# Performance work log

Measured on AMD Instinct MI355X. Metric: run time of the kernel, lower is better.

Reference implementation:

```python
import jax, jax.numpy as jnp
import numpy as np

H = 16          # num query heads
G = 4           # num kv heads (groups)
MAX_POS = 128   # max relative position


def setup_inputs() -> dict:
    key = jax.random.key(0)
    ks = jax.random.split(key, 6)
    B, T, D = 8, 1024, 1024
    hd = D // H
    s = 0.02
    return {
        "x": jax.random.normal(ks[0], (B, T, D), jnp.float32),
        "Wq": jax.random.normal(ks[1], (D, D), jnp.float32) * s,
        "Wk": jax.random.normal(ks[2], (hd * G, D), jnp.float32) * s,
        "Wv": jax.random.normal(ks[3], (hd * G, D), jnp.float32) * s,
        "Wo": jax.random.normal(ks[4], (D, D), jnp.float32) * s,
        "E": jax.random.normal(ks[5], (2 * MAX_POS - 1, hd), jnp.float32) * s,
    }


def reference(x, Wq, Wk, Wv, Wo, E):
    B, T, D = x.shape
    hd = D // H
    r = H // G  # kv repeat factor

    # projections (torch nn.Linear convention: y = x @ W.T)
    q = (x @ Wq.T).reshape(B, T, H, hd).transpose(0, 2, 1, 3)  # [B,H,T,hd]
    k = (x @ Wk.T).reshape(B, T, G, hd)                         # [B,T,G,hd]
    v = (x @ Wv.T).reshape(B, T, G, hd)

    # GQA: query head h uses kv group h // r  (matches repeat_interleave)
    k = jnp.repeat(k, r, axis=2).transpose(0, 2, 1, 3)  # [B,H,T,hd]
    v = jnp.repeat(v, r, axis=2).transpose(0, 2, 1, 3)  # [B,H,T,hd]

    q = q * (1.0 / hd) ** 0.5
    scores = jnp.einsum("bhqd,bhkd->bhqk", q, k)  # [B,H,T,T]

    # relative position bias: R[i,j] = E[clamp(j - i) + MAX_POS - 1]
    pos = jnp.arange(T)
    dist = jnp.clip(pos[None, :] - pos[:, None], -MAX_POS + 1, MAX_POS - 1) + MAX_POS - 1
    R = E[dist]  # [T,T,hd]
    # original einsum 'bhd,thd->bht' with q=[B*H, Tq, hd], R=[Tk, Tq, hd]:
    # bias[b,h,q,kpos] = sum_d q[b,h,q,d] * R[kpos, q, d]
    bias = jnp.einsum("bhqd,kqd->bhqk", q, R)
    scores = scores + bias

    attn = jax.nn.softmax(scores, axis=-1)
    out = jnp.einsum("bhqk,bhkd->bhqd", attn, v)         # [B,H,T,hd]
    out = out.transpose(0, 2, 1, 3).reshape(B, T, D)      # [B,T,D]
    return out @ Wo.T
```

## Files before the change

kernel.cpp:

```cpp
#include <hip/hip_runtime.h>
#include <hip/hip_bf16.h>
#include <cstdint>
#include <cstddef>

typedef __hip_bfloat16 bf16;
typedef __attribute__((ext_vector_type(8))) __bf16 bf16x8;
typedef __attribute__((ext_vector_type(4))) float floatx4;

#define GPTR(p) ((const __attribute__((address_space(1))) void*)(p))
#define LPTR(p) ((__attribute__((address_space(3))) void*)(p))

__device__ __forceinline__ floatx4 mfma16(bf16x8 a, bf16x8 b, floatx4 c) {
  return __builtin_amdgcn_mfma_f32_16x16x32_bf16(a, b, c, 0, 0, 0);
}

__global__ __launch_bounds__(256) void cvt_bf16(const float* __restrict__ in,
                                                bf16* __restrict__ out, int n4) {
  for (int i = blockIdx.x * 256 + threadIdx.x; i < n4; i += gridDim.x * 256) {
    float4 v = ((const float4*)in)[i];
    alignas(8) bf16 t[4] = {__float2bfloat16(v.x), __float2bfloat16(v.y),
                            __float2bfloat16(v.z), __float2bfloat16(v.w)};
    *(uint64_t*)(out + (size_t)i * 4) = *(const uint64_t*)t;
  }
}

__global__ __launch_bounds__(256) void gemm_qkv(
    const bf16* __restrict__ A, const bf16* __restrict__ Wq,
    const bf16* __restrict__ Wk, const bf16* __restrict__ Wv,
    bf16* __restrict__ qout, bf16* __restrict__ kout,
    bf16* __restrict__ vTout) {
  __shared__ alignas(16) bf16 As[128 * 32];
  __shared__ alignas(16) bf16 Bs[128 * 32];
  const int tid = threadIdx.x;
  const int lane = tid & 63;
  const int w = tid >> 6;
  const int wr = w >> 1, wc = w & 1;
  const int quad = lane >> 4, c = lane & 15;
  const int m0 = blockIdx.y * 128;
  const int nb = blockIdx.x;

  int mode, nloc;
  const bf16* Wp;
  if (nb < 8) {
    mode = 1; Wp = Wq + (size_t)nb * 128 * 1024; nloc = nb * 128;
  } else if (nb < 10) {
    mode = 2; Wp = Wk + (size_t)(nb - 8) * 128 * 1024; nloc = (nb - 8) * 128;
  } else {
    mode = 3; Wp = Wv + (size_t)(nb - 10) * 128 * 1024; nloc = (nb - 10) * 128;
  }

  const int i0 = tid, i1 = tid + 256;
  const bf16* ga0 = A + (size_t)(m0 + (i0 >> 2)) * 1024 + (i0 & 3) * 8;
  const bf16* ga1 = A + (size_t)(m0 + (i1 >> 2)) * 1024 + (i1 & 3) * 8;
  const bf16* gb0 = Wp + (size_t)(i0 >> 2) * 1024 + (i0 & 3) * 8;
  const bf16* gb1 = Wp + (size_t)(i1 >> 2) * 1024 + (i1 & 3) * 8;

  floatx4 acc[4][4] = {};

  for (int kt = 0; kt < 32; ++kt) {
    if (kt) __syncthreads();
    __builtin_amdgcn_global_load_lds(GPTR(ga0), LPTR(&As[i0 * 8]), 16, 0, 0);
    __builtin_amdgcn_global_load_lds(GPTR(ga1), LPTR(&As[i1 * 8]), 16, 0, 0);
    __builtin_amdgcn_global_load_lds(GPTR(gb0), LPTR(&Bs[i0 * 8]), 16, 0, 0);
    __builtin_amdgcn_global_load_lds(GPTR(gb1), LPTR(&Bs[i1 * 8]), 16, 0, 0);
    ga0 += 32; ga1 += 32; gb0 += 32; gb1 += 32;
    __syncthreads();
    bf16x8 af[4], bfr[4];
#pragma unroll
    for (int i = 0; i < 4; ++i)
      af[i] = *(const bf16x8*)&As[(wr * 64 + i * 16 + c) * 32 + quad * 8];
#pragma unroll
    for (int j = 0; j < 4; ++j)
      bfr[j] = *(const bf16x8*)&Bs[(wc * 64 + j * 16 + c) * 32 + quad * 8];
#pragma unroll
    for (int i = 0; i < 4; ++i)
#pragma unroll
      for (int j = 0; j < 4; ++j)
        acc[i][j] = mfma16(af[i], bfr[j], acc[i][j]);
  }

  if (mode == 3) {
#pragma unroll
    for (int i = 0; i < 4; ++i)
#pragma unroll
      for (int j = 0; j < 4; ++j) {
        int m = m0 + wr * 64 + i * 16 + quad * 4;
        int n = nloc + wc * 64 + j * 16 + c;
        int b = m >> 10, t = m & 1023, g = n >> 6, d = n & 63;
        alignas(8) bf16 tmp[4];
#pragma unroll
        for (int r = 0; r < 4; ++r) tmp[r] = __float2bfloat16(acc[i][j][r]);
        *(uint64_t*)(vTout + (((size_t)(b * 4 + g)) * 64 + d) * 1024 + t) =
            *(const uint64_t*)tmp;
      }
    return;
  }

  const float scale = (mode == 1) ? 0.125f : 1.0f;
#pragma unroll
  for (int i = 0; i < 4; ++i)
#pragma unroll
    for (int j = 0; j < 4; ++j)
#pragma unroll
      for (int r = 0; r < 4; ++r) {
        int m = m0 + wr * 64 + i * 16 + quad * 4 + r;
        int n = nloc + wc * 64 + j * 16 + c;
        int b = m >> 10, t = m & 1023;
        bf16 v = __float2bfloat16(acc[i][j][r] * scale);
        if (mode == 1) {
          int h = n >> 6;
          qout[(((size_t)(b * 16 + h)) * 1024 + t) * 64 + (n & 63)] = v;
        } else {
          int g = n >> 6;
          kout[(((size_t)(b * 4 + g)) * 1024 + t) * 64 + (n & 63)] = v;
        }
      }
}

__global__ __launch_bounds__(256) void gemm_o(const bf16* __restrict__ A,
                                              const bf16* __restrict__ W,
                                              float* __restrict__ out) {
  __shared__ alignas(16) bf16 As[128 * 32];
  __shared__ alignas(16) bf16 Bs[128 * 32];
  const int tid = threadIdx.x;
  const int lane = tid & 63;
  const int w = tid >> 6;
  const int wr = w >> 1, wc = w & 1;
  const int quad = lane >> 4, c = lane & 15;
  const int m0 = blockIdx.y * 128, n0 = blockIdx.x * 128;

  const int i0 = tid, i1 = tid + 256;
  const bf16* ga0 = A + (size_t)(m0 + (i0 >> 2)) * 1024 + (i0 & 3) * 8;
  const bf16* ga1 = A + (size_t)(m0 + (i1 >> 2)) * 1024 + (i1 & 3) * 8;
  const bf16* gb0 = W + (size_t)(n0 + (i0 >> 2)) * 1024 + (i0 & 3) * 8;
  const bf16* gb1 = W + (size_t)(n0 + (i1 >> 2)) * 1024 + (i1 & 3) * 8;

  floatx4 acc[4][4] = {};

  for (int kt = 0; kt < 32; ++kt) {
    if (kt) __syncthreads();
    __builtin_amdgcn_global_load_lds(GPTR(ga0), LPTR(&As[i0 * 8]), 16, 0, 0);
    __builtin_amdgcn_global_load_lds(GPTR(ga1), LPTR(&As[i1 * 8]), 16, 0, 0);
    __builtin_amdgcn_global_load_lds(GPTR(gb0), LPTR(&Bs[i0 * 8]), 16, 0, 0);
    __builtin_amdgcn_global_load_lds(GPTR(gb1), LPTR(&Bs[i1 * 8]), 16, 0, 0);
    ga0 += 32; ga1 += 32; gb0 += 32; gb1 += 32;
    __syncthreads();
    bf16x8 af[4], bfr[4];
#pragma unroll
    for (int i = 0; i < 4; ++i)
      af[i] = *(const bf16x8*)&As[(wr * 64 + i * 16 + c) * 32 + quad * 8];
#pragma unroll
    for (int j = 0; j < 4; ++j)
      bfr[j] = *(const bf16x8*)&Bs[(wc * 64 + j * 16 + c) * 32 + quad * 8];
#pragma unroll
    for (int i = 0; i < 4; ++i)
#pragma unroll
      for (int j = 0; j < 4; ++j)
        acc[i][j] = mfma16(af[i], bfr[j], acc[i][j]);
  }

#pragma unroll
  for (int i = 0; i < 4; ++i)
#pragma unroll
    for (int j = 0; j < 4; ++j)
#pragma unroll
      for (int r = 0; r < 4; ++r) {
        int m = m0 + wr * 64 + i * 16 + quad * 4 + r;
        int n = n0 + wc * 64 + j * 16 + c;
        out[(size_t)m * 1024 + n] = acc[i][j][r];
      }
}

__device__ __forceinline__ void stage_tile_swz(const bf16* __restrict__ g,
                                               int gstride, bf16* __restrict__ dst,
                                               int tid) {
#pragma unroll
  for (int s = 0; s < 2; ++s) {
    int f = s * 256 + tid;
    int r = f >> 3, cb = f & 7;
    int cbg = cb ^ (r & 7);
    __builtin_amdgcn_global_load_lds(GPTR(g + (size_t)r * gstride + cbg * 8),
                                     LPTR(dst + f * 8), 16, 0, 0);
  }
}

__device__ __forceinline__ bf16x8 read_frag_swz(const bf16* __restrict__ tile,
                                                int row, int cb) {
  return *(const bf16x8*)&tile[row * 64 + ((cb ^ (row & 7)) * 8)];
}

__global__ __launch_bounds__(256, 3) void attn_kernel(
    const bf16* __restrict__ q_ws, const bf16* __restrict__ k_ws,
    const bf16* __restrict__ vT, const float* __restrict__ E,
    bf16* __restrict__ out) {
  __shared__ alignas(16) bf16 qEl[64 * 264];
  __shared__ alignas(16) bf16 Ks[64 * 72];
  __shared__ alignas(16) bf16 Vs[64 * 64];
  const int tid = threadIdx.x;
  const int lane = tid & 63, w = tid >> 6;
  const int quad = lane >> 4, c = lane & 15;
  const int bh = blockIdx.y;
  const int b = bh >> 4, h = bh & 15, g = h >> 2;
  const int qb = blockIdx.x * 64 + w * 16;

  const bf16* qrow = q_ws + ((size_t)bh * 1024 + qb + c) * 64;
  bf16x8 qf0 = *(const bf16x8*)(qrow + quad * 8);
  bf16x8 qf1 = *(const bf16x8*)(qrow + 32 + quad * 8);

  for (int jn = 0; jn < 16; ++jn) {
    int er = jn * 16 + c;
    er = er > 254 ? 254 : er;
    const float* Ep = E + (size_t)er * 64;
    float4 e0 = *(const float4*)(Ep + quad * 8);
    float4 e1 = *(const float4*)(Ep + quad * 8 + 4);
    float4 e2 = *(const float4*)(Ep + 32 + quad * 8);
    float4 e3 = *(const float4*)(Ep + 32 + quad * 8 + 4);
    alignas(16) bf16 t0b[8] = {
        __float2bfloat16(e0.x), __float2bfloat16(e0.y), __float2bfloat16(e0.z),
        __float2bfloat16(e0.w), __float2bfloat16(e1.x), __float2bfloat16(e1.y),
        __float2bfloat16(e1.z), __float2bfloat16(e1.w)};
    alignas(16) bf16 t1b[8] = {
        __float2bfloat16(e2.x), __float2bfloat16(e2.y), __float2bfloat16(e2.z),
        __float2bfloat16(e2.w), __float2bfloat16(e3.x), __float2bfloat16(e3.y),
        __float2bfloat16(e3.z), __float2bfloat16(e3.w)};
    floatx4 a = {};
    a = mfma16(qf0, *(const bf16x8*)t0b, a);
    a = mfma16(qf1, *(const bf16x8*)t1b, a);
#pragma unroll
    for (int r = 0; r < 4; ++r)
      qEl[(w * 16 + quad * 4 + r) * 264 + jn * 16 + c] = __float2bfloat16(a[r]);
  }

  const bf16* rowE = qEl + (size_t)(w * 16 + c) * 264;
  bf16* rowP = Ks + (size_t)(w * 16 + c) * 72;
  float mrow = -1e30f, lrow = 0.f;
  floatx4 o[4] = {};
  const bf16* kbase = k_ws + (size_t)(b * 4 + g) * 1024 * 64;
  const bf16* vbase = vT + (size_t)(b * 4 + g) * 64 * 1024;
  float blo = 0.f, bhi = 0.f;

  for (int t0 = 0; t0 < 1024; t0 += 64) {
    stage_tile_swz(kbase + (size_t)t0 * 64, 64, Ks, tid);
    stage_tile_swz(vbase + t0, 1024, Vs, tid);
    __syncthreads();
    if (t0 == 0) {
      blo = __bfloat162float(rowE[254]);
      bhi = __bfloat162float(rowE[0]);
    }
    floatx4 S[4];
#pragma unroll
    for (int j = 0; j < 4; ++j) {
      bf16x8 kf0 = read_frag_swz(Ks, j * 16 + c, quad);
      bf16x8 kf1 = read_frag_swz(Ks, j * 16 + c, quad + 4);
      floatx4 z = {};
      z = mfma16(kf0, qf0, z);
      S[j] = mfma16(kf1, qf1, z);
    }
    const int dlt0 = qb + c - t0;
    if (t0 <= qb - 190) {
#pragma unroll
      for (int j = 0; j < 4; ++j)
#pragma unroll
        for (int r = 0; r < 4; ++r) S[j][r] += blo;
    } else if (t0 >= qb + 142) {
#pragma unroll
      for (int j = 0; j < 4; ++j)
#pragma unroll
        for (int r = 0; r < 4; ++r) S[j][r] += bhi;
    } else {
#pragma unroll
      for (int j = 0; j < 4; ++j)
#pragma unroll
        for (int r = 0; r < 4; ++r) {
          int dlt = dlt0 - j * 16 - quad * 4 - r;
          dlt = dlt > 127 ? 127 : (dlt < -127 ? -127 : dlt);
          S[j][r] += __bfloat162float(rowE[dlt + 127]);
        }
    }
    float mx = -1e30f;
#pragma unroll
    for (int j = 0; j < 4; ++j)
#pragma unroll
      for (int r = 0; r < 4; ++r) mx = fmaxf(mx, S[j][r]);
    mx = fmaxf(mx, __shfl_xor(mx, 16, 64));
    mx = fmaxf(mx, __shfl_xor(mx, 32, 64));
    float nm = fmaxf(mrow, mx);
    float alpha = __expf(mrow - nm);
    float rs = 0.f;
#pragma unroll
    for (int j = 0; j < 4; ++j)
#pragma unroll
      for (int r = 0; r < 4; ++r) {
        float p = __expf(S[j][r] - nm);
        S[j][r] = p;
        rs += p;
      }
    rs += __shfl_xor(rs, 16, 64);
    rs += __shfl_xor(rs, 32, 64);
    lrow = lrow * alpha + rs;
    mrow = nm;
    __syncthreads();
#pragma unroll
    for (int j = 0; j < 4; ++j) {
      alignas(8) bf16 tmp[4];
#pragma unroll
      for (int r = 0; r < 4; ++r) tmp[r] = __float2bfloat16(S[j][r]);
      *(uint64_t*)(rowP + j * 16 + quad * 4) = *(const uint64_t*)tmp;
    }
    float av[4];
#pragma unroll
    for (int r = 0; r < 4; ++r) av[r] = __shfl(alpha, quad * 4 + r, 64);
#pragma unroll
    for (int jj = 0; jj < 4; ++jj)
#pragma unroll
      for (int r = 0; r < 4; ++r) o[jj][r] *= av[r];
    __threadfence_block();
    __builtin_amdgcn_wave_barrier();
    bf16x8 pf0 = *(const bf16x8*)(rowP + quad * 8);
    bf16x8 pf1 = *(const bf16x8*)(rowP + 32 + quad * 8);
#pragma unroll
    for (int jj = 0; jj < 4; ++jj) {
      bf16x8 vf0 = read_frag_swz(Vs, jj * 16 + c, quad);
      bf16x8 vf1 = read_frag_swz(Vs, jj * 16 + c, quad + 4);
      o[jj] = mfma16(pf0, vf0, o[jj]);
      o[jj] = mfma16(pf1, vf1, o[jj]);
    }
    __syncthreads();
  }

  float lr4[4];
#pragma unroll
  for (int r = 0; r < 4; ++r) lr4[r] = __shfl(lrow, quad * 4 + r, 64);
#pragma unroll
  for (int jj = 0; jj < 4; ++jj)
#pragma unroll
    for (int r = 0; r < 4; ++r) {
      int qi = qb + quad * 4 + r;
      out[(((size_t)b * 1024 + qi) * 16 + h) * 64 + jj * 16 + c] =
          __float2bfloat16(o[jj][r] / lr4[r]);
    }
}

extern "C" void kernel_launch(void* const* d_in, const int* in_sizes, int n_in,
                              void* d_out, int out_size, void* d_ws,
                              size_t ws_size, hipStream_t stream) {
  const float* x = (const float*)d_in[0];
  const float* Wq = (const float*)d_in[1];
  const float* Wk = (const float*)d_in[2];
  const float* Wv = (const float*)d_in[3];
  const float* Wo = (const float*)d_in[4];
  const float* E = (const float*)d_in[5];

  char* ws = (char*)d_ws;
  bf16* q_ws = (bf16*)d_out;
  bf16* x_bf = (bf16*)((char*)d_out + (16ull << 20));
  bf16* k_ws = (bf16*)(ws);
  bf16* vT = (bf16*)(ws + (4ull << 20));
  bf16* attn = (bf16*)(ws + (8ull << 20));
  bf16* Wq_bf = (bf16*)(ws + (8ull << 20));
  bf16* Wk_bf = (bf16*)(ws + (10ull << 20));
  bf16* Wv_bf = (bf16*)(ws + (10ull << 20) + (512ull << 10));
  bf16* Wo_bf = (bf16*)(ws);
  float* outp = (float*)d_out;

  cvt_bf16<<<2048, 256, 0, stream>>>(x, x_bf, 2097152);
  cvt_bf16<<<1024, 256, 0, stream>>>(Wq, Wq_bf, 262144);
  cvt_bf16<<<256, 256, 0, stream>>>(Wk, Wk_bf, 65536);
  cvt_bf16<<<256, 256, 0, stream>>>(Wv, Wv_bf, 65536);
  gemm_qkv<<<dim3(12, 64), 256, 0, stream>>>(x_bf, Wq_bf, Wk_bf, Wv_bf,
                                             q_ws, k_ws, vT);
  attn_kernel<<<dim3(16, 128), 256, 0, stream>>>(q_ws, k_ws, vT, E, attn);
  cvt_bf16<<<1024, 256, 0, stream>>>(Wo, Wo_bf, 262144);
  gemm_o<<<dim3(8, 64), 256, 0, stream>>>(attn, Wo_bf, outp);
}
```

Before: 285.6 us.

## Load K/V fragments directly from global memory into registers, drop LDS staging

Replaces the shared-memory staging of K and V tiles (global_load_lds with swizzle plus block barriers) with direct per-wave global loads of MFMA fragments into registers. P now gets its own small LDS buffer and the per-iteration __syncthreads are removed, so waves run independently. The cost is that each of the four waves redundantly fetches the same K/V tiles from global/L2, and the uncoalesced row-strided 16-byte loads may raise memory traffic and latency.

```diff
diff --git a/kernel.cpp b/kernel.cpp
--- a/kernel.cpp
+++ b/kernel.cpp
@@ -171,31 +171,12 @@
       }
 }
 
-__device__ __forceinline__ void stage_tile_swz(const bf16* __restrict__ g,
-                                               int gstride, bf16* __restrict__ dst,
-                                               int tid) {
-#pragma unroll
-  for (int s = 0; s < 2; ++s) {
-    int f = s * 256 + tid;
-    int r = f >> 3, cb = f & 7;
-    int cbg = cb ^ (r & 7);
-    __builtin_amdgcn_global_load_lds(GPTR(g + (size_t)r * gstride + cbg * 8),
-                                     LPTR(dst + f * 8), 16, 0, 0);
-  }
-}
-
-__device__ __forceinline__ bf16x8 read_frag_swz(const bf16* __restrict__ tile,
-                                                int row, int cb) {
-  return *(const bf16x8*)&tile[row * 64 + ((cb ^ (row & 7)) * 8)];
-}
-
 __global__ __launch_bounds__(256, 3) void attn_kernel(
     const bf16* __restrict__ q_ws, const bf16* __restrict__ k_ws,
     const bf16* __restrict__ vT, const float* __restrict__ E,
     bf16* __restrict__ out) {
   __shared__ alignas(16) bf16 qEl[64 * 264];
-  __shared__ alignas(16) bf16 Ks[64 * 72];
-  __shared__ alignas(16) bf16 Vs[64 * 64];
+  __shared__ alignas(16) bf16 Ps[64 * 72];
   const int tid = threadIdx.x;
   const int lane = tid & 63, w = tid >> 6;
   const int quad = lane >> 4, c = lane & 15;
@@ -230,31 +211,38 @@
     for (int r = 0; r < 4; ++r)
       qEl[(w * 16 + quad * 4 + r) * 264 + jn * 16 + c] = __float2bfloat16(a[r]);
   }
+  __syncthreads();
 
   const bf16* rowE = qEl + (size_t)(w * 16 + c) * 264;
-  bf16* rowP = Ks + (size_t)(w * 16 + c) * 72;
+  bf16* rowP = Ps + (size_t)(w * 16 + c) * 72;
   float mrow = -1e30f, lrow = 0.f;
   floatx4 o[4] = {};
   const bf16* kbase = k_ws + (size_t)(b * 4 + g) * 1024 * 64;
   const bf16* vbase = vT + (size_t)(b * 4 + g) * 64 * 1024;
-  float blo = 0.f, bhi = 0.f;
+  const float blo = __bfloat162float(rowE[254]);
+  const float bhi = __bfloat162float(rowE[0]);
 
   for (int t0 = 0; t0 < 1024; t0 += 64) {
-    stage_tile_swz(kbase + (size_t)t0 * 64, 64, Ks, tid);
-    stage_tile_swz(vbase + t0, 1024, Vs, tid);
-    __syncthreads();
-    if (t0 == 0) {
-      blo = __bfloat162float(rowE[254]);
-      bhi = __bfloat162float(rowE[0]);
+    bf16x8 kf[4][2];
+#pragma unroll
+    for (int j = 0; j < 4; ++j) {
+      const bf16* kr = kbase + (size_t)(t0 + j * 16 + c) * 64 + quad * 8;
+      kf[j][0] = *(const bf16x8*)kr;
+      kf[j][1] = *(const bf16x8*)(kr + 32);
     }
     floatx4 S[4];
 #pragma unroll
     for (int j = 0; j < 4; ++j) {
-      bf16x8 kf0 = read_frag_swz(Ks, j * 16 + c, quad);
-      bf16x8 kf1 = read_frag_swz(Ks, j * 16 + c, quad + 4);
       floatx4 z = {};
-      z = mfma16(kf0, qf0, z);
-      S[j] = mfma16(kf1, qf1, z);
+      z = mfma16(kf[j][0], qf0, z);
+      S[j] = mfma16(kf[j][1], qf1, z);
+    }
+    bf16x8 vf[4][2];
+#pragma unroll
+    for (int jj = 0; jj < 4; ++jj) {
+      const bf16* vr = vbase + (size_t)(jj * 16 + c) * 1024 + t0 + quad * 8;
+      vf[jj][0] = *(const bf16x8*)vr;
+      vf[jj][1] = *(const bf16x8*)(vr + 32);
     }
     const int dlt0 = qb + c - t0;
     if (t0 <= qb - 190) {
@@ -299,7 +287,6 @@
     rs += __shfl_xor(rs, 32, 64);
     lrow = lrow * alpha + rs;
     mrow = nm;
-    __syncthreads();
 #pragma unroll
     for (int j = 0; j < 4; ++j) {
       alignas(8) bf16 tmp[4];
@@ -320,12 +307,9 @@
     bf16x8 pf1 = *(const bf16x8*)(rowP + 32 + quad * 8);
 #pragma unroll
     for (int jj = 0; jj < 4; ++jj) {
-      bf16x8 vf0 = read_frag_swz(Vs, jj * 16 + c, quad);
-      bf16x8 vf1 = read_frag_swz(Vs, jj * 16 + c, quad + 4);
-      o[jj] = mfma16(pf0, vf0, o[jj]);
-      o[jj] = mfma16(pf1, vf1, o[jj]);
-    }
-    __syncthreads();
+      o[jj] = mfma16(pf0, vf[jj][0], o[jj]);
+      o[jj] = mfma16(pf1, vf[jj][1], o[jj]);
+    }
   }
 
   float lr4[4];
```

Result: slower. 445.8 us (+56.1%).

## Double-buffer K/V tiles in attention loop to overlap loads with compute

Applied to the files above, without the earlier changes.

Splits K and V shared buffers into two ping-pong copies and issues the async global-to-LDS load of the next tile before computing on the current one, so memory latency overlaps the MFMA and softmax work. The first tile is prefetched before the positional-bias precompute, and the loop is manually unrolled by two to swap buffers. It also lowers the launch-bounds occupancy hint from 3 to 2 blocks per CU to fit the extra shared memory. The last iteration wraps around and prefetches tile 0 needlessly, adding a little redundant traffic.

```diff
diff --git a/kernel.cpp b/kernel.cpp
--- a/kernel.cpp
+++ b/kernel.cpp
@@ -189,19 +189,124 @@
   return *(const bf16x8*)&tile[row * 64 + ((cb ^ (row & 7)) * 8)];
 }
 
-__global__ __launch_bounds__(256, 3) void attn_kernel(
+__device__ __forceinline__ void attn_tile(
+    int t0, const bf16* __restrict__ kbase, const bf16* __restrict__ vbase,
+    bf16* __restrict__ curK, bf16* __restrict__ nxtK,
+    bf16* __restrict__ curV, bf16* __restrict__ nxtV,
+    const bf16* __restrict__ rowE, int qb, int tid, int w, int quad, int c,
+    bf16x8 qf0, bf16x8 qf1, float blo, float bhi, float& mrow, float& lrow,
+    floatx4 (&o)[4]) {
+  const int nt0 = (t0 + 64) & 1023;
+  stage_tile_swz(vbase + nt0, 1024, nxtV, tid);
+  stage_tile_swz(kbase + (size_t)nt0 * 64, 64, nxtK, tid);
+  floatx4 S[4];
+#pragma unroll
+  for (int j = 0; j < 4; ++j) {
+    bf16x8 kf0 = read_frag_swz(curK, j * 16 + c, quad);
+    bf16x8 kf1 = read_frag_swz(curK, j * 16 + c, quad + 4);
+    floatx4 z = {};
+    z = mfma16(kf0, qf0, z);
+    S[j] = mfma16(kf1, qf1, z);
+  }
+  const int dlt0 = qb + c - t0;
+  if (t0 <= qb - 190) {
+#pragma unroll
+    for (int j = 0; j < 4; ++j)
+#pragma unroll
+      for (int r = 0; r < 4; ++r) S[j][r] += blo;
+  } else if (t0 >= qb + 142) {
+#pragma unroll
+    for (int j = 0; j < 4; ++j)
+#pragma unroll
+      for (int r = 0; r < 4; ++r) S[j][r] += bhi;
+  } else {
+#pragma unroll
+    for (int j = 0; j < 4; ++j)
+#pragma unroll
+      for (int r = 0; r < 4; ++r) {
+        int dlt = dlt0 - j * 16 - quad * 4 - r;
+        dlt = dlt > 127 ? 127 : (dlt < -127 ? -127 : dlt);
+        S[j][r] += __bfloat162float(rowE[dlt + 127]);
+      }
+  }
+  float mx = -1e30f;
+#pragma unroll
+  for (int j = 0; j < 4; ++j)
+#pragma unroll
+    for (int r = 0; r < 4; ++r) mx = fmaxf(mx, S[j][r]);
+  mx = fmaxf(mx, __shfl_xor(mx, 16, 64));
+  mx = fmaxf(mx, __shfl_xor(mx, 32, 64));
+  float nm = fmaxf(mrow, mx);
+  float alpha = __expf(mrow - nm);
+  float rs = 0.f;
+#pragma unroll
+  for (int j = 0; j < 4; ++j)
+#pragma unroll
+    for (int r = 0; r < 4; ++r) {
+      float p = __expf(S[j][r] - nm);
+      S[j][r] = p;
+      rs += p;
+    }
+  rs += __shfl_xor(rs, 16, 64);
+  rs += __shfl_xor(rs, 32, 64);
+  lrow = lrow * alpha + rs;
+  mrow = nm;
+  __builtin_amdgcn_sched_barrier(0);
+  __builtin_amdgcn_s_barrier();
+  __builtin_amdgcn_sched_barrier(0);
+  bf16* rowP = curK + (size_t)(w * 16 + c) * 72;
+#pragma unroll
+  for (int j = 0; j < 4; ++j) {
+    alignas(8) bf16 tmp[4];
+#pragma unroll
+    for (int r = 0; r < 4; ++r) tmp[r] = __float2bfloat16(S[j][r]);
+    *(uint64_t*)(rowP + j * 16 + quad * 4) = *(const uint64_t*)tmp;
+  }
+  float av[4];
+#pragma unroll
+  for (int r = 0; r < 4; ++r) av[r] = __shfl(alpha, quad * 4 + r, 64);
+#pragma unroll
+  for (int jj = 0; jj < 4; ++jj)
+#pragma unroll
+    for (int r = 0; r < 4; ++r) o[jj][r] *= av[r];
+  __threadfence_block();
+  __builtin_amdgcn_wave_barrier();
+  bf16x8 pf0 = *(const bf16x8*)(rowP + quad * 8);
+  bf16x8 pf1 = *(const bf16x8*)(rowP + 32 + quad * 8);
+#pragma unroll
+  for (int jj = 0; jj < 4; ++jj) {
+    bf16x8 vf0 = read_frag_swz(curV, jj * 16 + c, quad);
+    bf16x8 vf1 = read_frag_swz(curV, jj * 16 + c, quad + 4);
+    o[jj] = mfma16(pf0, vf0, o[jj]);
+    o[jj] = mfma16(pf1, vf1, o[jj]);
+  }
+  asm volatile("s_waitcnt vmcnt(0)" ::: "memory");
+  __builtin_amdgcn_sched_barrier(0);
+  __builtin_amdgcn_s_barrier();
+  __builtin_amdgcn_sched_barrier(0);
+}
+
+__global__ __launch_bounds__(256, 2) void attn_kernel(
     const bf16* __restrict__ q_ws, const bf16* __restrict__ k_ws,
     const bf16* __restrict__ vT, const float* __restrict__ E,
     bf16* __restrict__ out) {
   __shared__ alignas(16) bf16 qEl[64 * 264];
-  __shared__ alignas(16) bf16 Ks[64 * 72];
-  __shared__ alignas(16) bf16 Vs[64 * 64];
+  __shared__ alignas(16) bf16 Ka[64 * 72];
+  __shared__ alignas(16) bf16 Kc[64 * 72];
+  __shared__ alignas(16) bf16 Va[64 * 64];
+  __shared__ alignas(16) bf16 Vc[64 * 64];
   const int tid = threadIdx.x;
   const int lane = tid & 63, w = tid >> 6;
   const int quad = lane >> 4, c = lane & 15;
   const int bh = blockIdx.y;
   const int b = bh >> 4, h = bh & 15, g = h >> 2;
   const int qb = blockIdx.x * 64 + w * 16;
+
+  const bf16* kbase = k_ws + (size_t)(b * 4 + g) * 1024 * 64;
+  const bf16* vbase = vT + (size_t)(b * 4 + g) * 64 * 1024;
+
+  stage_tile_swz(kbase, 64, Ka, tid);
+  stage_tile_swz(vbase, 1024, Va, tid);
 
   const bf16* qrow = q_ws + ((size_t)bh * 1024 + qb + c) * 64;
   bf16x8 qf0 = *(const bf16x8*)(qrow + quad * 8);
@@ -230,102 +335,20 @@
     for (int r = 0; r < 4; ++r)
       qEl[(w * 16 + quad * 4 + r) * 264 + jn * 16 + c] = __float2bfloat16(a[r]);
   }
+  __syncthreads();
 
   const bf16* rowE = qEl + (size_t)(w * 16 + c) * 264;
-  bf16* rowP = Ks + (size_t)(w * 16 + c) * 72;
   float mrow = -1e30f, lrow = 0.f;
   floatx4 o[4] = {};
-  const bf16* kbase = k_ws + (size_t)(b * 4 + g) * 1024 * 64;
-  const bf16* vbase = vT + (size_t)(b * 4 + g) * 64 * 1024;
-  float blo = 0.f, bhi = 0.f;
-
-  for (int t0 = 0; t0 < 1024; t0 += 64) {
-    stage_tile_swz(kbase + (size_t)t0 * 64, 64, Ks, tid);
-    stage_tile_swz(vbase + t0, 1024, Vs, tid);
-    __syncthreads();
-    if (t0 == 0) {
-      blo = __bfloat162float(rowE[254]);
-      bhi = __bfloat162float(rowE[0]);
-    }
-    floatx4 S[4];
-#pragma unroll
-    for (int j = 0; j < 4; ++j) {
-      bf16x8 kf0 = read_frag_swz(Ks, j * 16 + c, quad);
-      bf16x8 kf1 = read_frag_swz(Ks, j * 16 + c, quad + 4);
-      floatx4 z = {};
-      z = mfma16(kf0, qf0, z);
-      S[j] = mfma16(kf1, qf1, z);
-    }
-    const int dlt0 = qb + c - t0;
-    if (t0 <= qb - 190) {
-#pragma unroll
-      for (int j = 0; j < 4; ++j)
-#pragma unroll
-        for (int r = 0; r < 4; ++r) S[j][r] += blo;
-    } else if (t0 >= qb + 142) {
-#pragma unroll
-      for (int j = 0; j < 4; ++j)
-#pragma unroll
-        for (int r = 0; r < 4; ++r) S[j][r] += bhi;
-    } else {
-#pragma unroll
-      for (int j = 0; j < 4; ++j)
-#pragma unroll
-        for (int r = 0; r < 4; ++r) {
-          int dlt = dlt0 - j * 16 - quad * 4 - r;
-          dlt = dlt > 127 ? 127 : (dlt < -127 ? -127 : dlt);
-          S[j][r] += __bfloat162float(rowE[dlt + 127]);
-        }
-    }
-    float mx = -1e30f;
-#pragma unroll
-    for (int j = 0; j < 4; ++j)
-#pragma unroll
-      for (int r = 0; r < 4; ++r) mx = fmaxf(mx, S[j][r]);
-    mx = fmaxf(mx, __shfl_xor(mx, 16, 64));
-    mx = fmaxf(mx, __shfl_xor(mx, 32, 64));
-    float nm = fmaxf(mrow, mx);
-    float alpha = __expf(mrow - nm);
-    float rs = 0.f;
-#pragma unroll
-    for (int j = 0; j < 4; ++j)
-#pragma unroll
-      for (int r = 0; r < 4; ++r) {
-        float p = __expf(S[j][r] - nm);
-        S[j][r] = p;
-        rs += p;
-      }
-    rs += __shfl_xor(rs, 16, 64);
-    rs += __shfl_xor(rs, 32, 64);
-    lrow = lrow * alpha + rs;
-    mrow = nm;
-    __syncthreads();
-#pragma unroll
-    for (int j = 0; j < 4; ++j) {
-      alignas(8) bf16 tmp[4];
-#pragma unroll
-      for (int r = 0; r < 4; ++r) tmp[r] = __float2bfloat16(S[j][r]);
-      *(uint64_t*)(rowP + j * 16 + quad * 4) = *(const uint64_t*)tmp;
-    }
-    float av[4];
-#pragma unroll
-    for (int r = 0; r < 4; ++r) av[r] = __shfl(alpha, quad * 4 + r, 64);
-#pragma unroll
-    for (int jj = 0; jj < 4; ++jj)
-#pragma unroll
-      for (int r = 0; r < 4; ++r) o[jj][r] *= av[r];
-    __threadfence_block();
-    __builtin_amdgcn_wave_barrier();
-    bf16x8 pf0 = *(const bf16x8*)(rowP + quad * 8);
-    bf16x8 pf1 = *(const bf16x8*)(rowP + 32 + quad * 8);
-#pragma unroll
-    for (int jj = 0; jj < 4; ++jj) {
-      bf16x8 vf0 = read_frag_swz(Vs, jj * 16 + c, quad);
-      bf16x8 vf1 = read_frag_swz(Vs, jj * 16 + c, quad + 4);
-      o[jj] = mfma16(pf0, vf0, o[jj]);
-      o[jj] = mfma16(pf1, vf1, o[jj]);
-    }
-    __syncthreads();
+  const float blo = __bfloat162float(rowE[254]);
+  const float bhi = __bfloat162float(rowE[0]);
+
+#pragma unroll 1
+  for (int tp = 0; tp < 8; ++tp) {
+    attn_tile(tp * 128, kbase, vbase, Ka, Kc, Va, Vc, rowE, qb, tid, w, quad,
+              c, qf0, qf1, blo, bhi, mrow, lrow, o);
+    attn_tile(tp * 128 + 64, kbase, vbase, Kc, Ka, Vc, Va, rowE, qb, tid, w,
+              quad, c, qf0, qf1, blo, bhi, mrow, lrow, o);
   }
 
   float lr4[4];
```

New measurement: 293.9 us. +2.9%, slower.
